# Kernel tuning notes

Measured on AMD Instinct MI355X. Metric: run time of the kernel, lower is better.

Reference implementation:

```python
import jax, jax.numpy as jnp
import numpy as np

DIM = 512
CODEBOOK_SIZE = 8192
CODEBOOK_DIM = 13  # log2(8192)
CODEBOOK_SCALE = 1.0
DIVERSITY_GAMMA = 1.0
COMMIT_W = 0.25
ENTROPY_W = 0.1
EPS = 1e-5


def make_codebook():
    mask = 2 ** jnp.arange(CODEBOOK_DIM - 1, -1, -1)  # [13]
    codes = jnp.arange(CODEBOOK_SIZE)
    bits = ((codes[:, None] & mask) != 0).astype(jnp.float32)
    return bits * 2.0 * CODEBOOK_SCALE - CODEBOOK_SCALE  # [8192, 13]


def setup_inputs() -> dict:
    key = jax.random.key(0)
    k1, k2, k3, k4, k5 = jax.random.split(key, 5)
    x = jax.random.normal(k1, (4, 2048, DIM), dtype=jnp.float32)
    w_in = jax.random.normal(k2, (DIM, CODEBOOK_DIM), dtype=jnp.float32) * (DIM ** -0.5)
    b_in = jax.random.normal(k3, (CODEBOOK_DIM,), dtype=jnp.float32) * 0.01
    w_out = jax.random.normal(k4, (CODEBOOK_DIM, DIM), dtype=jnp.float32) * (CODEBOOK_DIM ** -0.5)
    b_out = jax.random.normal(k5, (DIM,), dtype=jnp.float32) * 0.01
    return {"x": x, "w_in": w_in, "b_in": b_in, "w_out": w_out, "b_out": b_out,
            "codebook": make_codebook()}


def reference(x, w_in, b_in, w_out, b_out, codebook):
    # project_in: [b, n, dim] -> [b, n, cd]
    h = jnp.einsum('bnd,dc->bnc', x, w_in) + b_in
    original_input = h

    # sign quantization
    quantized = jnp.where(h > 0, CODEBOOK_SCALE, -CODEBOOK_SCALE).astype(h.dtype)
    bit_mask = 2 ** jnp.arange(CODEBOOK_DIM - 1, -1, -1, dtype=jnp.int32)
    indices = jnp.sum((quantized > 0).astype(jnp.int32) * bit_mask, axis=-1)  # [b, n]

    # straight-through estimator (training branch)
    xq = h + jax.lax.stop_gradient(quantized - h)

    # entropy aux loss: affinity = -distance = 2 * <orig, codebook>
    logits = 2.0 * jnp.einsum('bnc,kc->bnk', original_input, codebook)  # [b, n, K]
    probs = jax.nn.softmax(logits, axis=-1)
    log_probs = jax.nn.log_softmax(logits + EPS, axis=-1)
    per_sample_entropy = -jnp.mean(jnp.sum(probs * log_probs, axis=-1))
    avg_probs = jnp.mean(probs.reshape(-1, CODEBOOK_SIZE), axis=0)
    codebook_entropy = -jnp.sum(avg_probs * jnp.log(avg_probs + EPS))
    entropy_aux_loss = 1.0 * per_sample_entropy - DIVERSITY_GAMMA * codebook_entropy

    # commitment loss
    commit_loss = jnp.mean((original_input - jax.lax.stop_gradient(quantized)) ** 2)

    # project_out
    out = jnp.einsum('bnc,cd->bnd', xq, w_out) + b_out

    aux_loss = entropy_aux_loss * ENTROPY_W + commit_loss * COMMIT_W
    return out, indices, aux_loss
```

## Files before the change

### kernel.cpp

```cpp
#include <hip/hip_runtime.h>
#include <math.h>

#define NTOK 8192
#define DIMV 512
#define CD 13
#define KSZ 8192
#define NPARTS 512
#define TPB 16

#define C_BYTES  ((size_t)NPARTS * KSZ * 4)
#define PC_OFF   C_BYTES
#define E_OFF    (PC_OFF + 4096)

__global__ __launch_bounds__(256) void ka_fused(const float* __restrict__ x,
                                                const float* __restrict__ w_in,
                                                const float* __restrict__ b_in,
                                                const float* __restrict__ w_out,
                                                const float* __restrict__ b_out,
                                                float* __restrict__ ws_C,
                                                float* __restrict__ ws_pc,
                                                float* __restrict__ outv,
                                                float* __restrict__ out_ind) {
  __shared__ __align__(16) float s_winT[CD * DIMV];
  __shared__ float sh[TPB][CD];
  __shared__ __align__(16) float sA[TPB][2][32];
  __shared__ __align__(16) float sB[TPB][128];
  __shared__ float s_cm[16], s_pe[16];
  int t = threadIdx.x;

  for (int d = t; d < DIMV; d += 256) {
#pragma unroll
    for (int c = 0; c < CD; ++c) s_winT[c * DIMV + d] = w_in[d * CD + c];
  }
  __syncthreads();

  int lane = t & 63;
  int wave = t >> 6;
  int l15 = lane & 15;
  int grp = lane >> 4;
  int tok = wave * 4 + grp;
  int n = blockIdx.x * TPB + tok;

  const float4* x4 = (const float4*)(x + (size_t)n * DIMV);

  float facc[CD];
#pragma unroll
  for (int c = 0; c < CD; ++c) facc[c] = 0.f;
#pragma unroll
  for (int j = 0; j < 8; ++j) {
    float4 xv = x4[l15 + j * 16];
    int dbase = (l15 + j * 16) * 4;
#pragma unroll
    for (int c = 0; c < CD; ++c) {
      const float4 wv = *(const float4*)&s_winT[c * DIMV + dbase];
      facc[c] += xv.x * wv.x + xv.y * wv.y + xv.z * wv.z + xv.w * wv.w;
    }
  }
  double acc[CD];
#pragma unroll
  for (int c = 0; c < CD; ++c) {
    double a = (double)facc[c];
    a += __shfl_xor(a, 1, 64);
    a += __shfl_xor(a, 2, 64);
    a += __shfl_xor(a, 4, 64);
    a += __shfl_xor(a, 8, 64);
    acc[c] = a + (double)b_in[c];
  }

  int idx = 0;
#pragma unroll
  for (int c = 0; c < CD; ++c) idx |= (acc[c] > 0.0 ? 1 : 0) << (12 - c);
  if (l15 == 0) out_ind[n] = (float)idx;

  float hv = 0.f;
#pragma unroll
  for (int c = 0; c < CD; ++c) if (l15 == c) hv = (float)acc[c];
  float cm = 0.f, pe = 0.f;
  if (l15 < CD) {
    sh[tok][l15] = hv;
    float a = fabsf(hv);
    float d1 = a - 1.f;
    cm = d1 * d1;
    float z = 4.f * a;
    float e = expf(-z);
    pe = log1pf(e) + z * e / (1.f + e);
  }
  cm += __shfl_xor(cm, 1, 64); pe += __shfl_xor(pe, 1, 64);
  cm += __shfl_xor(cm, 2, 64); pe += __shfl_xor(pe, 2, 64);
  cm += __shfl_xor(cm, 4, 64); pe += __shfl_xor(pe, 4, 64);
  cm += __shfl_xor(cm, 8, 64); pe += __shfl_xor(pe, 8, 64);
  if (l15 == 0) { s_cm[tok] = cm; s_pe[tok] = pe; }

  int dpos = lane * 4;
  int id2[4];
#pragma unroll
  for (int tt = 0; tt < 4; ++tt) id2[tt] = __shfl(idx, tt * 16, 64);
  float4 o[4][2];
  {
    float4 bo0 = *(const float4*)(b_out + dpos);
    float4 bo1 = *(const float4*)(b_out + dpos + 256);
#pragma unroll
    for (int tt = 0; tt < 4; ++tt) { o[tt][0] = bo0; o[tt][1] = bo1; }
  }
#pragma unroll
  for (int c = 0; c < CD; ++c) {
    const float4 w0 = *(const float4*)&w_out[c * DIMV + dpos];
    const float4 w1 = *(const float4*)&w_out[c * DIMV + dpos + 256];
#pragma unroll
    for (int tt = 0; tt < 4; ++tt) {
      float sgn = ((id2[tt] >> (12 - c)) & 1) ? 1.f : -1.f;
      o[tt][0].x = fmaf(sgn, w0.x, o[tt][0].x);
      o[tt][0].y = fmaf(sgn, w0.y, o[tt][0].y);
      o[tt][0].z = fmaf(sgn, w0.z, o[tt][0].z);
      o[tt][0].w = fmaf(sgn, w0.w, o[tt][0].w);
      o[tt][1].x = fmaf(sgn, w1.x, o[tt][1].x);
      o[tt][1].y = fmaf(sgn, w1.y, o[tt][1].y);
      o[tt][1].z = fmaf(sgn, w1.z, o[tt][1].z);
      o[tt][1].w = fmaf(sgn, w1.w, o[tt][1].w);
    }
  }
  int n0 = blockIdx.x * TPB + wave * 4;
#pragma unroll
  for (int tt = 0; tt < 4; ++tt) {
    float4* dst = (float4*)(outv + (size_t)(n0 + tt) * DIMV);
    dst[lane] = o[tt][0];
    dst[lane + 64] = o[tt][1];
  }

  __syncthreads();

  if (t == 0) {
    float C = 0.f, P = 0.f;
#pragma unroll
    for (int i = 0; i < 16; ++i) { C += s_cm[i]; P += s_pe[i]; }
    ws_pc[blockIdx.x * 2] = C;
    ws_pc[blockIdx.x * 2 + 1] = P;
  }

  for (int m = wave; m < TPB; m += 4) {
    float p[CD], q[CD];
#pragma unroll
    for (int c = 0; c < CD; ++c) {
      float hvv = sh[m][c];
      float e = expf(-4.f * hvv);
      float r = 1.f / (1.f + e);
      p[c] = r;
      q[c] = e * r;
    }
    float A = ((lane >> 5) & 1) ? p[0] : q[0];
    A *= ((lane >> 4) & 1) ? p[1] : q[1];
    A *= ((lane >> 3) & 1) ? p[2] : q[2];
    A *= ((lane >> 2) & 1) ? p[3] : q[3];
    A *= ((lane >> 1) & 1) ? p[4] : q[4];
    A *= (lane & 1) ? p[5] : q[5];
    sA[m][lane & 1][lane >> 1] = A;
    float Bb = ((lane >> 5) & 1) ? p[7] : q[7];
    Bb *= ((lane >> 4) & 1) ? p[8] : q[8];
    Bb *= ((lane >> 3) & 1) ? p[9] : q[9];
    Bb *= ((lane >> 2) & 1) ? p[10] : q[10];
    Bb *= ((lane >> 1) & 1) ? p[11] : q[11];
    Bb *= (lane & 1) ? p[12] : q[12];
    sB[m][lane] = q[6] * Bb;
    sB[m][64 + lane] = p[6] * Bb;
  }
  __syncthreads();

  int c2 = t >> 7;
  int klo = t & 127;
  float acc2[32];
#pragma unroll
  for (int j = 0; j < 32; ++j) acc2[j] = 0.f;
  for (int m = 0; m < TPB; ++m) {
    float Bv = sB[m][klo];
    const float4* A4 = (const float4*)&sA[m][c2][0];
#pragma unroll
    for (int jj = 0; jj < 8; ++jj) {
      float4 a = A4[jj];
      acc2[jj * 4 + 0] = fmaf(a.x, Bv, acc2[jj * 4 + 0]);
      acc2[jj * 4 + 1] = fmaf(a.y, Bv, acc2[jj * 4 + 1]);
      acc2[jj * 4 + 2] = fmaf(a.z, Bv, acc2[jj * 4 + 2]);
      acc2[jj * 4 + 3] = fmaf(a.w, Bv, acc2[jj * 4 + 3]);
    }
  }
  float* dst = ws_C + (size_t)blockIdx.x * KSZ;
#pragma unroll
  for (int j = 0; j < 32; ++j) dst[t + 256 * j] = acc2[j];
}

__global__ __launch_bounds__(256) void kb_cbent(const float* __restrict__ ws_C,
                                                float* __restrict__ ws_e) {
  __shared__ float red[256];
  int t = threadIdx.x;
  int sl = t & 31, pg = t >> 5;
  int s = blockIdx.x * 32 + sl;
  float a0 = 0.f, a1 = 0.f, a2 = 0.f, a3 = 0.f;
  for (int i = 0; i < 64; i += 4) {
    a0 += ws_C[(size_t)(pg + 8 * (i + 0)) * KSZ + s];
    a1 += ws_C[(size_t)(pg + 8 * (i + 1)) * KSZ + s];
    a2 += ws_C[(size_t)(pg + 8 * (i + 2)) * KSZ + s];
    a3 += ws_C[(size_t)(pg + 8 * (i + 3)) * KSZ + s];
  }
  red[t] = (a0 + a1) + (a2 + a3);
  __syncthreads();
  float contrib = 0.f;
  if (t < 32) {
    float v = red[t];
#pragma unroll
    for (int j = 1; j < 8; ++j) v += red[t + 32 * j];
    float avg = v * (1.f / (float)NTOK);
    contrib = -avg * logf(avg + 1e-5f);
  }
  if (t < 64) {
    contrib += __shfl_xor(contrib, 1, 64);
    contrib += __shfl_xor(contrib, 2, 64);
    contrib += __shfl_xor(contrib, 4, 64);
    contrib += __shfl_xor(contrib, 8, 64);
    contrib += __shfl_xor(contrib, 16, 64);
    if (t == 0) ws_e[blockIdx.x] = contrib;
  }
}

__global__ __launch_bounds__(256) void kc_final(const float* __restrict__ ws_pc,
                                                const float* __restrict__ ws_e,
                                                float* __restrict__ d_aux) {
  __shared__ float rc[256], rp[256], re[256];
  int t = threadIdx.x;
  float cm = 0.f, pe = 0.f;
  for (int i = t; i < 512; i += 256) { cm += ws_pc[2 * i]; pe += ws_pc[2 * i + 1]; }
  rc[t] = cm; rp[t] = pe; re[t] = ws_e[t];
  __syncthreads();
  if (t < 64) {
    float C = rc[t] + rc[t + 64] + rc[t + 128] + rc[t + 192];
    float P = rp[t] + rp[t + 64] + rp[t + 128] + rp[t + 192];
    float E = re[t] + re[t + 64] + re[t + 128] + re[t + 192];
    C += __shfl_xor(C, 1, 64); P += __shfl_xor(P, 1, 64); E += __shfl_xor(E, 1, 64);
    C += __shfl_xor(C, 2, 64); P += __shfl_xor(P, 2, 64); E += __shfl_xor(E, 2, 64);
    C += __shfl_xor(C, 4, 64); P += __shfl_xor(P, 4, 64); E += __shfl_xor(E, 4, 64);
    C += __shfl_xor(C, 8, 64); P += __shfl_xor(P, 8, 64); E += __shfl_xor(E, 8, 64);
    C += __shfl_xor(C, 16, 64); P += __shfl_xor(P, 16, 64); E += __shfl_xor(E, 16, 64);
    C += __shfl_xor(C, 32, 64); P += __shfl_xor(P, 32, 64); E += __shfl_xor(E, 32, 64);
    if (t == 0) {
      float commit = C * (1.f / (float)(NTOK * CD));
      float psE = P * (1.f / (float)NTOK);
      d_aux[0] = 0.1f * (psE - E) + 0.25f * commit;
    }
  }
}

extern "C" void kernel_launch(void* const* d_in, const int* in_sizes, int n_in,
                              void* d_out, int out_size, void* d_ws, size_t ws_size,
                              hipStream_t stream) {
  const float* x     = (const float*)d_in[0];
  const float* w_in  = (const float*)d_in[1];
  const float* b_in  = (const float*)d_in[2];
  const float* w_out = (const float*)d_in[3];
  const float* b_out = (const float*)d_in[4];

  float* outv = (float*)d_out;
  float* ind  = outv + (size_t)NTOK * DIMV;
  float* aux  = ind + NTOK;

  float* ws_C  = (float*)d_ws;
  float* ws_pc = (float*)((char*)d_ws + PC_OFF);
  float* ws_e  = (float*)((char*)d_ws + E_OFF);

  ka_fused<<<NTOK / TPB, 256, 0, stream>>>(x, w_in, b_in, w_out, b_out,
                                           ws_C, ws_pc, outv, ind);
  kb_cbent<<<256, 256, 0, stream>>>(ws_C, ws_e);
  kc_final<<<1, 256, 0, stream>>>(ws_pc, ws_e, aux);
}
```

Measured before the change: 40.98 us.

## Split avg-probs outer product into separate kernel and halve tokens per block

The fused kernel is split. The projection kernel now handles 8 tokens per block, using 32 lanes per token, and writes the pre-quantization values h to a workspace buffer. A new kernel reads h in groups of 16 tokens and computes the per-partition codebook probability sums. This shrinks the first kernel's shared memory and register use and doubles its grid, which may raise occupancy, at the cost of an extra launch and a global round-trip for h.

```diff
diff --git a/kernel.cpp b/kernel.cpp
--- a/kernel.cpp
+++ b/kernel.cpp
@@ -6,26 +6,24 @@
 #define CD 13
 #define KSZ 8192
 #define NPARTS 512
-#define TPB 16
+#define TPB 8
 
 #define C_BYTES  ((size_t)NPARTS * KSZ * 4)
 #define PC_OFF   C_BYTES
-#define E_OFF    (PC_OFF + 4096)
-
-__global__ __launch_bounds__(256) void ka_fused(const float* __restrict__ x,
-                                                const float* __restrict__ w_in,
-                                                const float* __restrict__ b_in,
-                                                const float* __restrict__ w_out,
-                                                const float* __restrict__ b_out,
-                                                float* __restrict__ ws_C,
-                                                float* __restrict__ ws_pc,
-                                                float* __restrict__ outv,
-                                                float* __restrict__ out_ind) {
+#define E_OFF    (PC_OFF + 8192)
+#define H_OFF    (E_OFF + 4096)
+
+__global__ __launch_bounds__(256) void ka_slim(const float* __restrict__ x,
+                                               const float* __restrict__ w_in,
+                                               const float* __restrict__ b_in,
+                                               const float* __restrict__ w_out,
+                                               const float* __restrict__ b_out,
+                                               float* __restrict__ ws_h,
+                                               float* __restrict__ ws_pc,
+                                               float* __restrict__ outv,
+                                               float* __restrict__ out_ind) {
   __shared__ __align__(16) float s_winT[CD * DIMV];
-  __shared__ float sh[TPB][CD];
-  __shared__ __align__(16) float sA[TPB][2][32];
-  __shared__ __align__(16) float sB[TPB][128];
-  __shared__ float s_cm[16], s_pe[16];
+  __shared__ float s_cm[TPB], s_pe[TPB];
   int t = threadIdx.x;
 
   for (int d = t; d < DIMV; d += 256) {
@@ -36,9 +34,9 @@
 
   int lane = t & 63;
   int wave = t >> 6;
-  int l15 = lane & 15;
-  int grp = lane >> 4;
-  int tok = wave * 4 + grp;
+  int l31 = lane & 31;
+  int grp = lane >> 5;
+  int tok = wave * 2 + grp;
   int n = blockIdx.x * TPB + tok;
 
   const float4* x4 = (const float4*)(x + (size_t)n * DIMV);
@@ -47,9 +45,9 @@
 #pragma unroll
   for (int c = 0; c < CD; ++c) facc[c] = 0.f;
 #pragma unroll
-  for (int j = 0; j < 8; ++j) {
-    float4 xv = x4[l15 + j * 16];
-    int dbase = (l15 + j * 16) * 4;
+  for (int j = 0; j < 4; ++j) {
+    float4 xv = x4[l31 + j * 32];
+    int dbase = (l31 + j * 32) * 4;
 #pragma unroll
     for (int c = 0; c < CD; ++c) {
       const float4 wv = *(const float4*)&s_winT[c * DIMV + dbase];
@@ -64,20 +62,21 @@
     a += __shfl_xor(a, 2, 64);
     a += __shfl_xor(a, 4, 64);
     a += __shfl_xor(a, 8, 64);
+    a += __shfl_xor(a, 16, 64);
     acc[c] = a + (double)b_in[c];
   }
 
   int idx = 0;
 #pragma unroll
   for (int c = 0; c < CD; ++c) idx |= (acc[c] > 0.0 ? 1 : 0) << (12 - c);
-  if (l15 == 0) out_ind[n] = (float)idx;
+  if (l31 == 0) out_ind[n] = (float)idx;
 
   float hv = 0.f;
 #pragma unroll
-  for (int c = 0; c < CD; ++c) if (l15 == c) hv = (float)acc[c];
+  for (int c = 0; c < CD; ++c) if (l31 == c) hv = (float)acc[c];
   float cm = 0.f, pe = 0.f;
-  if (l15 < CD) {
-    sh[tok][l15] = hv;
+  if (l31 < CD) {
+    ws_h[(size_t)n * CD + l31] = hv;
     float a = fabsf(hv);
     float d1 = a - 1.f;
     cm = d1 * d1;
@@ -89,25 +88,26 @@
   cm += __shfl_xor(cm, 2, 64); pe += __shfl_xor(pe, 2, 64);
   cm += __shfl_xor(cm, 4, 64); pe += __shfl_xor(pe, 4, 64);
   cm += __shfl_xor(cm, 8, 64); pe += __shfl_xor(pe, 8, 64);
-  if (l15 == 0) { s_cm[tok] = cm; s_pe[tok] = pe; }
+  cm += __shfl_xor(cm, 16, 64); pe += __shfl_xor(pe, 16, 64);
+  if (l31 == 0) { s_cm[tok] = cm; s_pe[tok] = pe; }
 
   int dpos = lane * 4;
-  int id2[4];
-#pragma unroll
-  for (int tt = 0; tt < 4; ++tt) id2[tt] = __shfl(idx, tt * 16, 64);
-  float4 o[4][2];
+  int id2[2];
+  id2[0] = __shfl(idx, 0, 64);
+  id2[1] = __shfl(idx, 32, 64);
+  float4 o[2][2];
   {
     float4 bo0 = *(const float4*)(b_out + dpos);
     float4 bo1 = *(const float4*)(b_out + dpos + 256);
 #pragma unroll
-    for (int tt = 0; tt < 4; ++tt) { o[tt][0] = bo0; o[tt][1] = bo1; }
+    for (int tt = 0; tt < 2; ++tt) { o[tt][0] = bo0; o[tt][1] = bo1; }
   }
 #pragma unroll
   for (int c = 0; c < CD; ++c) {
     const float4 w0 = *(const float4*)&w_out[c * DIMV + dpos];
     const float4 w1 = *(const float4*)&w_out[c * DIMV + dpos + 256];
 #pragma unroll
-    for (int tt = 0; tt < 4; ++tt) {
+    for (int tt = 0; tt < 2; ++tt) {
       float sgn = ((id2[tt] >> (12 - c)) & 1) ? 1.f : -1.f;
       o[tt][0].x = fmaf(sgn, w0.x, o[tt][0].x);
       o[tt][0].y = fmaf(sgn, w0.y, o[tt][0].y);
@@ -119,29 +119,42 @@
       o[tt][1].w = fmaf(sgn, w1.w, o[tt][1].w);
     }
   }
-  int n0 = blockIdx.x * TPB + wave * 4;
-#pragma unroll
-  for (int tt = 0; tt < 4; ++tt) {
+  int n0 = blockIdx.x * TPB + wave * 2;
+#pragma unroll
+  for (int tt = 0; tt < 2; ++tt) {
     float4* dst = (float4*)(outv + (size_t)(n0 + tt) * DIMV);
     dst[lane] = o[tt][0];
     dst[lane + 64] = o[tt][1];
   }
 
   __syncthreads();
-
   if (t == 0) {
     float C = 0.f, P = 0.f;
 #pragma unroll
-    for (int i = 0; i < 16; ++i) { C += s_cm[i]; P += s_pe[i]; }
+    for (int i = 0; i < TPB; ++i) { C += s_cm[i]; P += s_pe[i]; }
     ws_pc[blockIdx.x * 2] = C;
     ws_pc[blockIdx.x * 2 + 1] = P;
   }
-
-  for (int m = wave; m < TPB; m += 4) {
+}
+
+__global__ __launch_bounds__(256) void kd_avgp(const float* __restrict__ ws_h,
+                                               float* __restrict__ ws_C) {
+  __shared__ float sh_f[16 * CD];
+  __shared__ __align__(16) float sA[16][2][32];
+  __shared__ __align__(16) float sB[16][128];
+  int t = threadIdx.x;
+  int lane = t & 63;
+  int wave = t >> 6;
+
+  for (int g = t; g < 16 * CD; g += 256)
+    sh_f[g] = ws_h[(size_t)blockIdx.x * (16 * CD) + g];
+  __syncthreads();
+
+  for (int m = wave; m < 16; m += 4) {
     float p[CD], q[CD];
 #pragma unroll
     for (int c = 0; c < CD; ++c) {
-      float hvv = sh[m][c];
+      float hvv = sh_f[m * CD + c];
       float e = expf(-4.f * hvv);
       float r = 1.f / (1.f + e);
       p[c] = r;
@@ -170,7 +183,7 @@
   float acc2[32];
 #pragma unroll
   for (int j = 0; j < 32; ++j) acc2[j] = 0.f;
-  for (int m = 0; m < TPB; ++m) {
+  for (int m = 0; m < 16; ++m) {
     float Bv = sB[m][klo];
     const float4* A4 = (const float4*)&sA[m][c2][0];
 #pragma unroll
@@ -226,7 +239,7 @@
   __shared__ float rc[256], rp[256], re[256];
   int t = threadIdx.x;
   float cm = 0.f, pe = 0.f;
-  for (int i = t; i < 512; i += 256) { cm += ws_pc[2 * i]; pe += ws_pc[2 * i + 1]; }
+  for (int i = t; i < 1024; i += 256) { cm += ws_pc[2 * i]; pe += ws_pc[2 * i + 1]; }
   rc[t] = cm; rp[t] = pe; re[t] = ws_e[t];
   __syncthreads();
   if (t < 64) {
@@ -263,9 +276,11 @@
   float* ws_C  = (float*)d_ws;
   float* ws_pc = (float*)((char*)d_ws + PC_OFF);
   float* ws_e  = (float*)((char*)d_ws + E_OFF);
-
-  ka_fused<<<NTOK / TPB, 256, 0, stream>>>(x, w_in, b_in, w_out, b_out,
-                                           ws_C, ws_pc, outv, ind);
+  float* ws_h  = (float*)((char*)d_ws + H_OFF);
+
+  ka_slim<<<NTOK / TPB, 256, 0, stream>>>(x, w_in, b_in, w_out, b_out,
+                                          ws_h, ws_pc, outv, ind);
+  kd_avgp<<<NPARTS, 256, 0, stream>>>(ws_h, ws_C);
   kb_cbent<<<256, 256, 0, stream>>>(ws_C, ws_e);
   kc_final<<<1, 256, 0, stream>>>(ws_pc, ws_e, aux);
 }
```

Result: slower. 46.02 us (+12.3%).
